# Performance work log

Hardware: AMD Instinct MI355X
Metric: run time of the kernel (lower is better)

## Reference

```python
import jax, jax.numpy as jnp
import numpy as np

MIN_NORM = 1e-15
BALL_EPS = 1e-5  # projection margin for the Poincare ball


def _tanh(x):
    return jnp.tanh(jnp.clip(x, -15.0, 15.0))


def _artanh(x):
    return jnp.arctanh(jnp.clip(x, -1.0 + 1e-5, 1.0 - 1e-5))


def givens_rotations(r, x):
    # r, x: (N, d) with d even -> (N, d)
    g = r.reshape(r.shape[0], -1, 2)
    g = g / jnp.maximum(jnp.linalg.norm(g, axis=-1, keepdims=True), MIN_NORM)
    xp = x.reshape(x.shape[0], -1, 2)
    swap = jnp.concatenate([-xp[..., 1:], xp[..., :1]], axis=-1)
    return (g[..., :1] * xp + g[..., 1:] * swap).reshape(r.shape[0], -1)


def givens_reflection(r, x):
    g = r.reshape(r.shape[0], -1, 2)
    g = g / jnp.maximum(jnp.linalg.norm(g, axis=-1, keepdims=True), MIN_NORM)
    xp = x.reshape(x.shape[0], -1, 2)
    a = jnp.concatenate([xp[..., :1], -xp[..., 1:]], axis=-1)
    b = jnp.concatenate([xp[..., 1:], xp[..., :1]], axis=-1)
    return (g[..., :1] * a + g[..., 1:] * b).reshape(r.shape[0], -1)


def expmap0(u, c):
    sqrt_c = jnp.sqrt(c)
    u_norm = jnp.maximum(jnp.linalg.norm(u, axis=-1, keepdims=True), MIN_NORM)
    return _tanh(sqrt_c * u_norm) * u / (sqrt_c * u_norm)


def mobius_add(x, y, c):
    x2 = jnp.sum(x * x, -1, keepdims=True)
    y2 = jnp.sum(y * y, -1, keepdims=True)
    xy = jnp.sum(x * y, -1, keepdims=True)
    num = (1 + 2 * c * xy + c * y2) * x + (1 - c * x2) * y
    denom = 1 + 2 * c * xy + c * c * x2 * y2
    return num / jnp.maximum(denom, MIN_NORM)


def project(x, c):
    norm = jnp.maximum(jnp.linalg.norm(x, axis=-1, keepdims=True), MIN_NORM)
    maxnorm = (1.0 - BALL_EPS) / jnp.sqrt(c)
    return jnp.where(norm > maxnorm, x / norm * maxnorm, x)


def hyp_distance_multi_c_bmm(x, v, c):
    # x: (nc, cs, d) queries; v: (nc, ns, d) candidates; c: (nc, cs, 1) curvatures
    sqrt_c = jnp.sqrt(c)                                              # (nc, cs, 1)
    vnorm = jnp.linalg.norm(v, axis=-1, keepdims=True).transpose(0, 2, 1)  # (nc, 1, ns)
    xv = jnp.einsum('bcd,bnd->bcn', x, v) / vnorm                     # (nc, cs, ns)
    gamma = _tanh(sqrt_c * vnorm) / sqrt_c                            # (nc, cs, ns)
    x2 = jnp.sum(x * x, -1, keepdims=True)                            # (nc, cs, 1)
    c1 = 1 - 2 * c * gamma * xv + c * gamma ** 2
    c2 = 1 - c * x2
    num = jnp.sqrt(jnp.maximum(c1 ** 2 * x2 + c2 ** 2 * gamma ** 2 - 2 * c1 * c2 * gamma * xv, 0.0))
    denom = 1 - 2 * c * gamma * xv + c ** 2 * gamma ** 2 * x2
    dist = _artanh(sqrt_c * num / jnp.maximum(denom, MIN_NORM))
    return 2 * dist / sqrt_c                                          # (nc, cs, ns)


def setup_inputs() -> dict:
    key = jax.random.key(0)
    nc, cs, ns, d = 16, 1024, 1024, 512
    B = nc * cs
    ks = jax.random.split(key, 8)
    return {
        'head': jax.random.normal(ks[0], (B, d), jnp.float32),
        'head_bias': jax.random.normal(ks[1], (B, 1), jnp.float32),
        'rel': jax.random.normal(ks[2], (B, d), jnp.float32),
        'rel_diag': jax.random.normal(ks[3], (B, 2 * d), jnp.float32),
        'curvature': jax.random.normal(ks[4], (B, 1), jnp.float32),
        'context': jax.random.normal(ks[5], (B, d), jnp.float32),
        'scale': jnp.full((1,), 1.0 / np.sqrt(d), jnp.float32),
        'tail': jax.random.normal(ks[6], (nc * ns, d), jnp.float32),
        'tail_bias': jax.random.normal(ks[7], (nc * ns, 1), jnp.float32),
        'chunk_size': cs,
        'neg_sample_size': ns,
    }


def reference(head, head_bias, rel, rel_diag, curvature, context, scale, tail,
              tail_bias, chunk_size, neg_sample_size):
    num_chunk = head.shape[0] // chunk_size
    d = head.shape[-1]
    c = jax.nn.softplus(curvature)                                    # (B, 1)
    rot_mat, ref_mat = jnp.split(rel_diag, 2, axis=-1)
    rot_q = givens_rotations(rot_mat, head)[:, None, :]               # (B, 1, d)
    ref_q = givens_reflection(ref_mat, head)[:, None, :]              # (B, 1, d)
    cands = jnp.concatenate([ref_q, rot_q], axis=1)                   # (B, 2, d)
    att_w = jax.nn.softmax(
        jnp.sum(context[:, None, :] * cands * scale, -1, keepdims=True), axis=1)
    att_q = jnp.sum(att_w * cands, axis=1)                            # (B, d)
    lhs = expmap0(att_q, c)
    rel_h = expmap0(rel, c)
    res = project(mobius_add(lhs, rel_h, c), c)                       # (B, d)
    x = res.reshape(num_chunk, chunk_size, d)
    v = tail.reshape(num_chunk, neg_sample_size, d)
    c3 = c.reshape(num_chunk, chunk_size, 1)
    dist = hyp_distance_multi_c_bmm(x, v, c3)                         # (nc, cs, ns)
    score = (-dist ** 2
             + head_bias.reshape(num_chunk, chunk_size, 1)
             + tail_bias.reshape(num_chunk, 1, neg_sample_size))
    return score
```

## Files before the change

kernel.cpp:

```cpp
#include <hip/hip_runtime.h>
#include <math.h>

#define DEV static __device__ __forceinline__

constexpr float MIN_NORM = 1e-15f;
constexpr float BALL_EPS = 1e-5f;
constexpr int D = 512;

typedef float f32x4 __attribute__((ext_vector_type(4)));
typedef short short8v __attribute__((ext_vector_type(8)));
typedef unsigned short ushort8v __attribute__((ext_vector_type(8)));

DEV float rcpf_(float x) { return __builtin_amdgcn_rcpf(x); }
DEV float rsqf_(float x) { return __builtin_amdgcn_rsqf(x); }

DEV float tanh_over_a_pos(float a) {
    const float e = __expf(-2.0f * a);
    return (1.0f - e) * rcpf_((1.0f + e) * fmaxf(a, 1e-20f));
}

DEV unsigned short f2bf(float f) {
    unsigned int u = __float_as_uint(f);
    u = (u + 0x7FFFu + ((u >> 16) & 1u)) >> 16;
    return (unsigned short)u;
}
DEV float bf2f(unsigned short h) { return __uint_as_float(((unsigned int)h) << 16); }

DEV void write_packed_row(unsigned short* pack, size_t nrow, int row,
                          int lane, ushort8v hi, ushort8v lo)
{
    const int kb  = lane >> 2;
    const int cch = lane & 3;
    const int rx  = row & 7;
    unsigned short* dst = pack + ((size_t)kb * nrow + row) * 64;
    *(ushort8v*)(dst + ((cch ^ rx) * 8))       = hi;
    *(ushort8v*)(dst + (((cch + 4) ^ rx) * 8)) = lo;
}

__global__ __launch_bounds__(256)
void prep_kernel(const float* __restrict__ head,
                 const float* __restrict__ rel,
                 const float* __restrict__ rel_diag,
                 const float* __restrict__ curvature,
                 const float* __restrict__ context,
                 const float* __restrict__ scale_p,
                 const float* __restrict__ tail,
                 unsigned short* __restrict__ packA,
                 unsigned short* __restrict__ packB,
                 float* __restrict__ row_x2,
                 float* __restrict__ row_c,
                 float* __restrict__ row_sc,
                 float* __restrict__ vnorm,
                 int B, int T)
{
    const int lane = threadIdx.x & 63;
    const int base = lane * 8;
    const int wid  = blockIdx.x * 4 + (threadIdx.x >> 6);
    const int r0   = wid * 2;

    if (r0 >= B) {
        const int tr = r0 - B;
        float v[2][8];
#pragma unroll
        for (int rr = 0; rr < 2; ++rr) {
            const size_t off = (size_t)(tr + rr) * D + base;
            *(float4*)&v[rr][0] = *(const float4*)(tail + off);
            *(float4*)&v[rr][4] = *(const float4*)(tail + off + 4);
        }
        float s[2] = {0.f, 0.f};
        ushort8v hi[2], lo[2];
#pragma unroll
        for (int rr = 0; rr < 2; ++rr)
#pragma unroll
            for (int e = 0; e < 8; ++e) {
                s[rr] += v[rr][e] * v[rr][e];
                const unsigned short hb_ = f2bf(v[rr][e]);
                hi[rr][e] = hb_;
                lo[rr][e] = f2bf(v[rr][e] - bf2f(hb_));
            }
#pragma unroll
        for (int o = 32; o > 0; o >>= 1)
#pragma unroll
            for (int rr = 0; rr < 2; ++rr)
                s[rr] += __shfl_xor(s[rr], o, 64);
#pragma unroll
        for (int rr = 0; rr < 2; ++rr) {
            write_packed_row(packB, (size_t)T, tr + rr, lane, hi[rr], lo[rr]);
            if (lane == 0) vnorm[tr + rr] = sqrtf(s[rr]);
        }
        return;
    }

    float hv[2][8], rv[2][8], gv[2][8], fv[2][8], cxv[2][8];
#pragma unroll
    for (int rr = 0; rr < 2; ++rr) {
        const size_t roff = (size_t)(r0 + rr) * D + base;
        const size_t doff = (size_t)(r0 + rr) * 2 * D + base;
        *(float4*)&hv[rr][0]  = *(const float4*)(head + roff);
        *(float4*)&hv[rr][4]  = *(const float4*)(head + roff + 4);
        *(float4*)&rv[rr][0]  = *(const float4*)(rel + roff);
        *(float4*)&rv[rr][4]  = *(const float4*)(rel + roff + 4);
        *(float4*)&gv[rr][0]  = *(const float4*)(rel_diag + doff);
        *(float4*)&gv[rr][4]  = *(const float4*)(rel_diag + doff + 4);
        *(float4*)&fv[rr][0]  = *(const float4*)(rel_diag + doff + D);
        *(float4*)&fv[rr][4]  = *(const float4*)(rel_diag + doff + D + 4);
        *(float4*)&cxv[rr][0] = *(const float4*)(context + roff);
        *(float4*)&cxv[rr][4] = *(const float4*)(context + roff + 4);
    }

    float rq[2][8], rf[2][8];
#pragma unroll
    for (int rr = 0; rr < 2; ++rr)
#pragma unroll
        for (int p = 0; p < 4; ++p) {
            const float x0 = hv[rr][2*p], x1 = hv[rr][2*p+1];
            float g0 = gv[rr][2*p], g1 = gv[rr][2*p+1];
            const float gi = rsqf_(fmaxf(g0*g0 + g1*g1, 1e-30f));
            g0 *= gi; g1 *= gi;
            rq[rr][2*p]   = g0*x0 - g1*x1;
            rq[rr][2*p+1] = g0*x1 + g1*x0;
            float f0 = fv[rr][2*p], f1 = fv[rr][2*p+1];
            const float fi = rsqf_(fmaxf(f0*f0 + f1*f1, 1e-30f));
            f0 *= fi; f1 *= fi;
            rf[rr][2*p]   = f0*x0 + f1*x1;
            rf[rr][2*p+1] = f1*x0 - f0*x1;
        }

    float s[2][8];
#pragma unroll
    for (int rr = 0; rr < 2; ++rr) {
#pragma unroll
        for (int k = 0; k < 8; ++k) s[rr][k] = 0.f;
#pragma unroll
        for (int e = 0; e < 8; ++e) {
            s[rr][0] += cxv[rr][e]*rf[rr][e];   s[rr][1] += cxv[rr][e]*rq[rr][e];
            s[rr][2] += rv[rr][e]*rv[rr][e];    s[rr][3] += rf[rr][e]*rv[rr][e];
            s[rr][4] += rq[rr][e]*rv[rr][e];    s[rr][5] += rf[rr][e]*rf[rr][e];
            s[rr][6] += rq[rr][e]*rq[rr][e];    s[rr][7] += rf[rr][e]*rq[rr][e];
        }
    }
#pragma unroll
    for (int o = 32; o > 0; o >>= 1)
#pragma unroll
        for (int rr = 0; rr < 2; ++rr)
#pragma unroll
            for (int k = 0; k < 8; ++k)
                s[rr][k] += __shfl_xor(s[rr][k], o, 64);

    const float sc = scale_p[0];
    float pre[2][8], r2p[2];
    float cS[2], sqcS[2];
#pragma unroll
    for (int rr = 0; rr < 2; ++rr) {
        const float cu = curvature[r0 + rr];
        const float c  = fmaxf(cu, 0.0f) + __logf(1.0f + __expf(-fabsf(cu)));
        const float sqc = sqrtf(c);
        cS[rr] = c; sqcS[rr] = sqc;

        const float a0 = s[rr][0] * sc, a1 = s[rr][1] * sc;
        const float mx = fmaxf(a0, a1);
        const float e0 = __expf(a0 - mx), e1 = __expf(a1 - mx);
        const float w0 = e0 * rcpf_(e0 + e1);
        const float w1 = 1.0f - w0;

        const float att2    = fmaxf(w0*w0*s[rr][5] + 2.0f*w0*w1*s[rr][7] + w1*w1*s[rr][6], 0.0f);
        const float attdrel = w0*s[rr][3] + w1*s[rr][4];
        const float u_att = fmaxf(sqrtf(att2), MIN_NORM);
        const float u_rel = fmaxf(sqrtf(s[rr][2]), MIN_NORM);

        const float kl = tanh_over_a_pos(sqc * u_att);
        const float kr = tanh_over_a_pos(sqc * u_rel);

        const float x2 = kl*kl*att2;
        const float y2 = kr*kr*s[rr][2];
        const float xy = kl*kr*attdrel;

        const float Am  = 1.0f + 2.0f*c*xy + c*y2;
        const float Bm  = 1.0f - c*x2;
        const float inv_den = rcpf_(fmaxf(1.0f + 2.0f*c*xy + c*c*x2*y2, MIN_NORM));

        r2p[rr] = 0.f;
#pragma unroll
        for (int e = 0; e < 8; ++e) {
            const float attq = w0*rf[rr][e] + w1*rq[rr][e];
            pre[rr][e] = (Am*kl*attq + Bm*kr*rv[rr][e]) * inv_den;
            r2p[rr] += pre[rr][e]*pre[rr][e];
        }
    }
#pragma unroll
    for (int o = 32; o > 0; o >>= 1)
#pragma unroll
        for (int rr = 0; rr < 2; ++rr)
            r2p[rr] += __shfl_xor(r2p[rr], o, 64);

#pragma unroll
    for (int rr = 0; rr < 2; ++rr) {
        const float nrm  = fmaxf(sqrtf(r2p[rr]), MIN_NORM);
        const float maxn = (1.0f - BALL_EPS) * rcpf_(sqcS[rr]);
        const float psc  = (nrm > maxn) ? (maxn * rcpf_(nrm)) : 1.0f;

        ushort8v hi, lo;
#pragma unroll
        for (int e = 0; e < 8; ++e) {
            const float o = pre[rr][e] * psc;
            const unsigned short hb_ = f2bf(o);
            hi[e] = hb_;
            lo[e] = f2bf(o - bf2f(hb_));
        }
        write_packed_row(packA, (size_t)B, r0 + rr, lane, hi, lo);

        if (lane == 0) {
            row_x2[r0 + rr] = r2p[rr] * psc * psc;
            row_c[r0 + rr]  = cS[rr];
            row_sc[r0 + rr] = sqcS[rr];
        }
    }
}

__global__ __launch_bounds__(512, 2)
void score_kernel(const unsigned short* __restrict__ packA,
                  const unsigned short* __restrict__ packB,
                  const float* __restrict__ vnorm,
                  const float* __restrict__ row_x2,
                  const float* __restrict__ row_c,
                  const float* __restrict__ row_sc,
                  const float* __restrict__ head_bias,
                  const float* __restrict__ tail_bias,
                  float* __restrict__ out,
                  int cs, int ns, int nrowA, int nrowB)
{
    extern __shared__ __align__(16) char smem[];

    const int orig = blockIdx.x;
    const int wg = (orig & 7) * 32 + (orig >> 3);
    const int bz = wg >> 4;
    const int by = (wg >> 2) & 3;
    const int bx = wg & 3;
    const int m0 = by * 256;
    const int n0 = bx * 256;

    const int tid  = threadIdx.x;
    const int lane = tid & 63;
    const int w    = tid >> 6;
    const int wr   = w >> 2, wn = w & 3;
    const int lrow = lane & 15, lg = lane >> 4;

    f32x4 acc[8][4];
#pragma unroll
    for (int i = 0; i < 8; ++i)
#pragma unroll
        for (int j = 0; j < 4; ++j) acc[i][j] = f32x4{0.f, 0.f, 0.f, 0.f};

    const int xr = (lg ^ (lrow & 7)) * 16;
    const int baseA = (wr * 128 + lrow) * 128 + xr;
    const int baseB = 32768 + (wn * 64 + lrow) * 128 + xr;

    const int s16 = (tid & 255) * 16;
    const int shi = tid >> 8;

    const char* gA = (const char*)packA + (size_t)(bz * cs + m0) * 128;
    const char* gB = (const char*)packB + (size_t)(bz * ns + n0) * 128;
    const size_t strA = (size_t)nrowA * 128;
    const size_t strB = (size_t)nrowB * 128;

#define GLL(srcp, dstp)                                                        \
    __builtin_amdgcn_global_load_lds(                                          \
        (const __attribute__((address_space(1))) unsigned int*)(srcp),         \
        (__attribute__((address_space(3))) unsigned int*)(dstp), 16, 0, 0)

#define STAGE(dstbase, srcpanel, off0, sstr)                                   \
    do { const int o_ = (off0) + s16 + shi * (sstr);                           \
         GLL((srcpanel) + o_, (dstbase) + o_); } while (0)

#define STAGE_ALL(dstslot, srcA, srcB)                                         \
    do {                                                                       \
        STAGE(dstslot, srcA, 0, 4096);      STAGE(dstslot, srcA, 16384, 4096); \
        STAGE(dstslot, srcA, 8192, 4096);   STAGE(dstslot, srcA, 24576, 4096); \
        STAGE((dstslot)+32768, srcB, 0, 8192);                                 \
        STAGE((dstslot)+32768, srcB, 16384, 8192);                             \
        STAGE((dstslot)+32768, srcB, 4096, 8192);                              \
        STAGE((dstslot)+32768, srcB, 20480, 8192);                             \
    } while (0)

#define RD(p, off) (*(const short8v*)((p) + (off)))
#define MFMA_(A_, B_, C_) __builtin_amdgcn_mfma_f32_16x16x32_bf16(A_, B_, C_, 0, 0, 0)

#define QUAD(MOFF, NOFF)                                                       \
    do {                                                                       \
        _Pragma("unroll") for (int mm = 0; mm < 4; ++mm)                       \
        _Pragma("unroll") for (int nn = 0; nn < 2; ++nn)                       \
            acc[(MOFF)+mm][(NOFF)+nn] = MFMA_(ah[mm], bh[(NOFF)+nn], acc[(MOFF)+mm][(NOFF)+nn]); \
        _Pragma("unroll") for (int mm = 0; mm < 4; ++mm)                       \
        _Pragma("unroll") for (int nn = 0; nn < 2; ++nn)                       \
            acc[(MOFF)+mm][(NOFF)+nn] = MFMA_(ah[mm], bl[(NOFF)+nn], acc[(MOFF)+mm][(NOFF)+nn]); \
        _Pragma("unroll") for (int mm = 0; mm < 4; ++mm)                       \
        _Pragma("unroll") for (int nn = 0; nn < 2; ++nn)                       \
            acc[(MOFF)+mm][(NOFF)+nn] = MFMA_(al[mm], bh[(NOFF)+nn], acc[(MOFF)+mm][(NOFF)+nn]); \
    } while (0)

#define BAR()   __builtin_amdgcn_s_barrier()
#define VM0()   asm volatile("s_waitcnt vmcnt(0)" ::: "memory")

    STAGE_ALL(smem, gA, gB);
    VM0();
    BAR();

    short8v ah[4], al[4], bh[4], bl[4];

#pragma unroll 1
    for (int t = 0; t < 16; ++t) {
        char* cur = smem + (t & 1) * 65536;
        char* oth = smem + ((t + 1) & 1) * 65536;

        if (t < 15)
            STAGE_ALL(oth, gA + (size_t)(t + 1) * strA, gB + (size_t)(t + 1) * strB);

#pragma unroll
        for (int m = 0; m < 4; ++m) {
            ah[m] = RD(cur, baseA + m * 2048);
            al[m] = RD(cur, (baseA ^ 64) + m * 2048);
        }
#pragma unroll
        for (int n = 0; n < 2; ++n) {
            bh[n] = RD(cur, baseB + n * 2048);
            bl[n] = RD(cur, (baseB ^ 64) + n * 2048);
        }
        QUAD(0, 0);
#pragma unroll
        for (int n = 2; n < 4; ++n) {
            bh[n] = RD(cur, baseB + n * 2048);
            bl[n] = RD(cur, (baseB ^ 64) + n * 2048);
        }
        QUAD(0, 2);
#pragma unroll
        for (int m = 0; m < 4; ++m) {
            ah[m] = RD(cur, baseA + 8192 + m * 2048);
            al[m] = RD(cur, (baseA ^ 64) + 8192 + m * 2048);
        }
        QUAD(4, 2);
        QUAD(4, 0);

        VM0();
        BAR();
    }

    const int nbase = n0 + wn * 64 + lrow;
    float rvn[4], vnv[4], tb[4];
#pragma unroll
    for (int j = 0; j < 4; ++j) {
        const int gn = bz * ns + nbase + j * 16;
        const float vn = vnorm[gn];
        vnv[j] = vn;
        rvn[j] = 1.0f / vn;
        tb[j]  = tail_bias[gn];
    }
#pragma unroll
    for (int i = 0; i < 8; ++i) {
#pragma unroll
        for (int q = 0; q < 4; ++q) {
            const int gm = bz * cs + m0 + wr * 128 + i * 16 + lg * 4 + q;
            const float x2  = row_x2[gm];
            const float cc  = row_c[gm];
            const float scq = row_sc[gm];
            const float hb  = head_bias[gm];
            const float rscq = 1.0f / scq;
            float* orow = out + (size_t)gm * ns + nbase;
#pragma unroll
            for (int j = 0; j < 4; ++j) {
                const float xv = acc[i][j][q] * rvn[j];
                float xx = fminf(scq * vnv[j], 15.0f);
                const float ey = __expf(2.0f * xx);
                const float g  = (1.0f - 2.0f / (ey + 1.0f)) * rscq;
                const float c1 = 1.0f - 2.0f*cc*g*xv + cc*g*g;
                const float c2 = 1.0f - cc*x2;
                const float num = sqrtf(fmaxf(c1*c1*x2 + c2*c2*g*g - 2.0f*c1*c2*g*xv, 0.0f));
                const float den = fmaxf(1.0f - 2.0f*cc*g*xv + cc*cc*g*g*x2, MIN_NORM);
                float tt = scq * num * __builtin_amdgcn_rcpf(den);
                tt = fminf(tt, 1.0f - 1e-5f);
                const float ath = 0.5f * __logf((1.0f + tt) * __builtin_amdgcn_rcpf(1.0f - tt));
                const float dist = 2.0f * rscq * ath;
                orow[j * 16] = -dist * dist + hb + tb[j];
            }
        }
    }
#undef GLL
#undef STAGE
#undef STAGE_ALL
#undef RD
#undef MFMA_
#undef QUAD
#undef BAR
#undef VM0
}

extern "C" void kernel_launch(void* const* d_in, const int* in_sizes, int n_in,
                              void* d_out, int out_size, void* d_ws, size_t ws_size,
                              hipStream_t stream)
{
    const float* head      = (const float*)d_in[0];
    const float* head_bias = (const float*)d_in[1];
    const float* rel       = (const float*)d_in[2];
    const float* rel_diag  = (const float*)d_in[3];
    const float* curvature = (const float*)d_in[4];
    const float* context   = (const float*)d_in[5];
    const float* scale     = (const float*)d_in[6];
    const float* tail      = (const float*)d_in[7];
    const float* tail_bias = (const float*)d_in[8];

    const int B  = in_sizes[1];
    const int T  = in_sizes[8];
    const int ns = out_size / B;
    const int nc = T / ns;
    const int cs = B / nc;

    unsigned short* packA = (unsigned short*)d_ws;
    unsigned short* packB = packA + (size_t)16 * B * 64;
    float* row_x2 = (float*)(packB + (size_t)16 * T * 64);
    float* row_c  = row_x2 + B;
    float* row_sc = row_c + B;
    float* vnormb = row_sc + B;

    prep_kernel<<<(B + T) / 8, 256, 0, stream>>>(head, rel, rel_diag, curvature,
                                                 context, scale, tail, packA, packB,
                                                 row_x2, row_c, row_sc, vnormb, B, T);

    (void)hipFuncSetAttribute((const void*)score_kernel,
                              hipFuncAttributeMaxDynamicSharedMemorySize, 131072);
    const int nblk = (ns / 256) * (cs / 256) * nc;
    score_kernel<<<nblk, 512, 131072, stream>>>(packA, packB, vnormb, row_x2, row_c,
                                                row_sc, head_bias, tail_bias,
                                                (float*)d_out, cs, ns, B, T);
}
```

Before: 126.6 us.

## Shrink score GEMM tile to 128x128 with 256 threads and static LDS

Changes the score kernel's block tile from 256x256 (512 threads, 128KB dynamic LDS) to 128x128 (256 threads, 64KB static double-buffered LDS), quadrupling the number of blocks. Each wave now computes a 64x64 subtile with 4x4 accumulators, and the staging and MFMA loops are simplified to match. The aim is more blocks per CU and better spread of work across the GPU's compute units. The cost is lower data reuse per block, so more global and LDS traffic for the same output.

```diff
diff --git a/kernel.cpp b/kernel.cpp
--- a/kernel.cpp
+++ b/kernel.cpp
@@ -217,7 +217,7 @@
     }
 }
 
-__global__ __launch_bounds__(512, 2)
+__global__ __launch_bounds__(256, 2)
 void score_kernel(const unsigned short* __restrict__ packA,
                   const unsigned short* __restrict__ packB,
                   const float* __restrict__ vnorm,
@@ -229,79 +229,63 @@
                   float* __restrict__ out,
                   int cs, int ns, int nrowA, int nrowB)
 {
-    extern __shared__ __align__(16) char smem[];
+    __shared__ __align__(16) char smem[2][32768];
 
     const int orig = blockIdx.x;
-    const int wg = (orig & 7) * 32 + (orig >> 3);
-    const int bz = wg >> 4;
-    const int by = (wg >> 2) & 3;
-    const int bx = wg & 3;
-    const int m0 = by * 256;
-    const int n0 = bx * 256;
+    const int wg = (orig & 7) * 128 + (orig >> 3);
+    const int bz = wg >> 6;
+    const int by = (wg >> 3) & 7;
+    const int bx = wg & 7;
+    const int m0 = by * 128;
+    const int n0 = bx * 128;
 
     const int tid  = threadIdx.x;
     const int lane = tid & 63;
     const int w    = tid >> 6;
-    const int wr   = w >> 2, wn = w & 3;
+    const int wr   = w >> 1, wc = w & 1;
     const int lrow = lane & 15, lg = lane >> 4;
 
-    f32x4 acc[8][4];
-#pragma unroll
-    for (int i = 0; i < 8; ++i)
+    f32x4 acc[4][4];
+#pragma unroll
+    for (int i = 0; i < 4; ++i)
 #pragma unroll
         for (int j = 0; j < 4; ++j) acc[i][j] = f32x4{0.f, 0.f, 0.f, 0.f};
 
     const int xr = (lg ^ (lrow & 7)) * 16;
-    const int baseA = (wr * 128 + lrow) * 128 + xr;
-    const int baseB = 32768 + (wn * 64 + lrow) * 128 + xr;
-
-    const int s16 = (tid & 255) * 16;
-    const int shi = tid >> 8;
+    const int baseA = (wr * 64 + lrow) * 128 + xr;
+    const int baseB = 16384 + (wc * 64 + lrow) * 128 + xr;
 
     const char* gA = (const char*)packA + (size_t)(bz * cs + m0) * 128;
     const char* gB = (const char*)packB + (size_t)(bz * ns + n0) * 128;
     const size_t strA = (size_t)nrowA * 128;
     const size_t strB = (size_t)nrowB * 128;
+    const int t16 = tid * 16;
 
 #define GLL(srcp, dstp)                                                        \
     __builtin_amdgcn_global_load_lds(                                          \
         (const __attribute__((address_space(1))) unsigned int*)(srcp),         \
         (__attribute__((address_space(3))) unsigned int*)(dstp), 16, 0, 0)
 
-#define STAGE(dstbase, srcpanel, off0, sstr)                                   \
-    do { const int o_ = (off0) + s16 + shi * (sstr);                           \
-         GLL((srcpanel) + o_, (dstbase) + o_); } while (0)
-
 #define STAGE_ALL(dstslot, srcA, srcB)                                         \
     do {                                                                       \
-        STAGE(dstslot, srcA, 0, 4096);      STAGE(dstslot, srcA, 16384, 4096); \
-        STAGE(dstslot, srcA, 8192, 4096);   STAGE(dstslot, srcA, 24576, 4096); \
-        STAGE((dstslot)+32768, srcB, 0, 8192);                                 \
-        STAGE((dstslot)+32768, srcB, 16384, 8192);                             \
-        STAGE((dstslot)+32768, srcB, 4096, 8192);                              \
-        STAGE((dstslot)+32768, srcB, 20480, 8192);                             \
+        _Pragma("unroll")                                                      \
+        for (int p_ = 0; p_ < 4; ++p_) {                                       \
+            const int o_ = p_ * 4096 + t16;                                    \
+            GLL((srcA) + o_, (dstslot) + o_);                                  \
+        }                                                                      \
+        _Pragma("unroll")                                                      \
+        for (int p_ = 0; p_ < 4; ++p_) {                                       \
+            const int o_ = p_ * 4096 + t16;                                    \
+            GLL((srcB) + o_, (dstslot) + 16384 + o_);                          \
+        }                                                                      \
     } while (0)
 
 #define RD(p, off) (*(const short8v*)((p) + (off)))
 #define MFMA_(A_, B_, C_) __builtin_amdgcn_mfma_f32_16x16x32_bf16(A_, B_, C_, 0, 0, 0)
-
-#define QUAD(MOFF, NOFF)                                                       \
-    do {                                                                       \
-        _Pragma("unroll") for (int mm = 0; mm < 4; ++mm)                       \
-        _Pragma("unroll") for (int nn = 0; nn < 2; ++nn)                       \
-            acc[(MOFF)+mm][(NOFF)+nn] = MFMA_(ah[mm], bh[(NOFF)+nn], acc[(MOFF)+mm][(NOFF)+nn]); \
-        _Pragma("unroll") for (int mm = 0; mm < 4; ++mm)                       \
-        _Pragma("unroll") for (int nn = 0; nn < 2; ++nn)                       \
-            acc[(MOFF)+mm][(NOFF)+nn] = MFMA_(ah[mm], bl[(NOFF)+nn], acc[(MOFF)+mm][(NOFF)+nn]); \
-        _Pragma("unroll") for (int mm = 0; mm < 4; ++mm)                       \
-        _Pragma("unroll") for (int nn = 0; nn < 2; ++nn)                       \
-            acc[(MOFF)+mm][(NOFF)+nn] = MFMA_(al[mm], bh[(NOFF)+nn], acc[(MOFF)+mm][(NOFF)+nn]); \
-    } while (0)
-
 #define BAR()   __builtin_amdgcn_s_barrier()
 #define VM0()   asm volatile("s_waitcnt vmcnt(0)" ::: "memory")
 
-    STAGE_ALL(smem, gA, gB);
+    STAGE_ALL(&smem[0][0], gA, gB);
     VM0();
     BAR();
 
@@ -309,8 +293,8 @@
 
 #pragma unroll 1
     for (int t = 0; t < 16; ++t) {
-        char* cur = smem + (t & 1) * 65536;
-        char* oth = smem + ((t + 1) & 1) * 65536;
+        char* cur = &smem[t & 1][0];
+        char* oth = &smem[(t + 1) & 1][0];
 
         if (t < 15)
             STAGE_ALL(oth, gA + (size_t)(t + 1) * strA, gB + (size_t)(t + 1) * strB);
@@ -321,30 +305,32 @@
             al[m] = RD(cur, (baseA ^ 64) + m * 2048);
         }
 #pragma unroll
-        for (int n = 0; n < 2; ++n) {
+        for (int n = 0; n < 4; ++n) {
             bh[n] = RD(cur, baseB + n * 2048);
             bl[n] = RD(cur, (baseB ^ 64) + n * 2048);
         }
-        QUAD(0, 0);
-#pragma unroll
-        for (int n = 2; n < 4; ++n) {
-            bh[n] = RD(cur, baseB + n * 2048);
-            bl[n] = RD(cur, (baseB ^ 64) + n * 2048);
-        }
-        QUAD(0, 2);
-#pragma unroll
-        for (int m = 0; m < 4; ++m) {
-            ah[m] = RD(cur, baseA + 8192 + m * 2048);
-            al[m] = RD(cur, (baseA ^ 64) + 8192 + m * 2048);
-        }
-        QUAD(4, 2);
-        QUAD(4, 0);
+
+#pragma unroll
+        for (int m = 0; m < 4; ++m)
+#pragma unroll
+            for (int n = 0; n < 4; ++n)
+                acc[m][n] = MFMA_(ah[m], bh[n], acc[m][n]);
+#pragma unroll
+        for (int m = 0; m < 4; ++m)
+#pragma unroll
+            for (int n = 0; n < 4; ++n)
+                acc[m][n] = MFMA_(ah[m], bl[n], acc[m][n]);
+#pragma unroll
+        for (int m = 0; m < 4; ++m)
+#pragma unroll
+            for (int n = 0; n < 4; ++n)
+                acc[m][n] = MFMA_(al[m], bh[n], acc[m][n]);
 
         VM0();
         BAR();
     }
 
-    const int nbase = n0 + wn * 64 + lrow;
+    const int nbase = n0 + wc * 64 + lrow;
     float rvn[4], vnv[4], tb[4];
 #pragma unroll
     for (int j = 0; j < 4; ++j) {
@@ -355,10 +341,10 @@
         tb[j]  = tail_bias[gn];
     }
 #pragma unroll
-    for (int i = 0; i < 8; ++i) {
+    for (int i = 0; i < 4; ++i) {
 #pragma unroll
         for (int q = 0; q < 4; ++q) {
-            const int gm = bz * cs + m0 + wr * 128 + i * 16 + lg * 4 + q;
+            const int gm = bz * cs + m0 + wr * 64 + i * 16 + lg * 4 + q;
             const float x2  = row_x2[gm];
             const float cc  = row_c[gm];
             const float scq = row_sc[gm];
@@ -384,11 +370,9 @@
         }
     }
 #undef GLL
-#undef STAGE
 #undef STAGE_ALL
 #undef RD
 #undef MFMA_
-#undef QUAD
 #undef BAR
 #undef VM0
 }
@@ -424,10 +408,8 @@
                                                  context, scale, tail, packA, packB,
                                                  row_x2, row_c, row_sc, vnormb, B, T);
 
-    (void)hipFuncSetAttribute((const void*)score_kernel,
-                              hipFuncAttributeMaxDynamicSharedMemorySize, 131072);
-    const int nblk = (ns / 256) * (cs / 256) * nc;
-    score_kernel<<<nblk, 512, 131072, stream>>>(packA, packB, vnormb, row_x2, row_c,
-                                                row_sc, head_bias, tail_bias,
-                                                (float*)d_out, cs, ns, B, T);
-}
+    const int nblk = (ns / 128) * (cs / 128) * nc;
+    score_kernel<<<nblk, 256, 0, stream>>>(packA, packB, vnormb, row_x2, row_c,
+                                           row_sc, head_bias, tail_bias,
+                                           (float*)d_out, cs, ns, B, T);
+}
```

After: 130.1 us. 1.03x slower.
